# Optimization experiments

Hardware: AMD Instinct MI355X
Metric: run time of the kernel (lower is better)

Reference implementation:

```python
import jax, jax.numpy as jnp
import numpy as np

B, S, K, N, G = 4, 2048, 4096, 11008, 128  # batch, seq, in_features, out_features, groupsize


def setup_inputs() -> dict:
    key = jax.random.key(0)
    k1, k2, k3, k4 = jax.random.split(key, 4)
    x = jax.random.normal(k1, (B, S, K), dtype=jnp.float32)
    # unpacked int4 codes in [0, 16)
    weight_q = jax.random.randint(k2, (N, K), 0, 16, dtype=jnp.int32)
    # groupwise scales (positive, small) and zeros, packed as [K//G, N, 2]
    scales = jax.random.uniform(k3, (K // G, N), dtype=jnp.float32) * 0.02 + 1e-3
    zeros = jax.random.normal(k4, (K // G, N), dtype=jnp.float32) * 0.1
    scales_and_zeros = jnp.stack([scales, zeros], axis=-1)  # [K//G, N, 2]
    return {"x": x, "weight_q": weight_q, "scales_and_zeros": scales_and_zeros}


def reference(x, weight_q, scales_and_zeros):
    # Dequantize groupwise: w[n,k] = (q[n,k] - 8) * scale[k//G, n] + zero[k//G, n]
    scales = scales_and_zeros[..., 0].T  # [N, K//G]
    zeros = scales_and_zeros[..., 1].T   # [N, K//G]
    q = weight_q.astype(x.dtype).reshape(N, K // G, G)  # [N, K//G, G]
    w = (q - 8.0) * scales[:, :, None] + zeros[:, :, None]  # fused dequant
    w = w.reshape(N, K)
    # y[b,s,n] = sum_k x[b,s,k] * w[n,k]
    return jnp.einsum("bsk,nk->bsn", x, w)
```

## Files before the change

kernel.cpp:

```cpp
#include <hip/hip_runtime.h>
#include <stdint.h>


typedef __attribute__((ext_vector_type(8))) short short8;
typedef __attribute__((ext_vector_type(4))) float float4v;
typedef __attribute__((ext_vector_type(4))) int int4v;
typedef __attribute__((ext_vector_type(2))) float float2v;
typedef __attribute__((ext_vector_type(4))) unsigned short ushort4v;

static constexpr int M_ = 8192;
static constexpr int K_ = 4096;
static constexpr int N_ = 11008;
static constexpr int NKT = K_ / 64;

__device__ __forceinline__ unsigned short f2bf(float f) {
    union { float f; uint32_t u; } v;
    v.f = f;
    uint32_t u = v.u;
    u += 0x7fffu + ((u >> 16) & 1u);
    return (unsigned short)(u >> 16);
}

__device__ __forceinline__ void gload16(const void* g, void* l) {
    __builtin_amdgcn_global_load_lds(
        (const __attribute__((address_space(1))) uint32_t*)g,
        (__attribute__((address_space(3))) uint32_t*)l, 16, 0, 0);
}

__global__ __launch_bounds__(256) void cvt_x_kernel(const float* __restrict__ X,
                                                    unsigned short* __restrict__ Xb) {
    const int i = blockIdx.x * 256 + threadIdx.x;
    const float4v a = ((const float4v*)X)[2 * (size_t)i];
    const float4v b = ((const float4v*)X)[2 * (size_t)i + 1];
    short8 o;
    #pragma unroll
    for (int j = 0; j < 4; ++j) o[j] = (short)f2bf(a[j]);
    #pragma unroll
    for (int j = 0; j < 4; ++j) o[4 + j] = (short)f2bf(b[j]);
    ((short8*)Xb)[(size_t)i] = o;
}

__global__ __launch_bounds__(256) void deq_w_kernel(const int* __restrict__ Q,
                                                    const float* __restrict__ SZ,
                                                    unsigned short* __restrict__ Wb) {
    const int i = blockIdx.x * 256 + threadIdx.x;
    const int n = i >> 9;
    const int c = i & 511;
    const int k0 = c * 8;
    const int g = k0 >> 7;
    const float2v sz = *(const float2v*)(SZ + ((size_t)g * N_ + n) * 2);
    const float s = sz[0], z = sz[1];
    const int4v q0 = *(const int4v*)(Q + (size_t)n * K_ + k0);
    const int4v q1 = *(const int4v*)(Q + (size_t)n * K_ + k0 + 4);
    short8 o;
    #pragma unroll
    for (int j = 0; j < 4; ++j) o[j] = (short)f2bf((float)(q0[j] - 8) * s + z);
    #pragma unroll
    for (int j = 0; j < 4; ++j) o[4 + j] = (short)f2bf((float)(q1[j] - 8) * s + z);
    ((short8*)Wb)[(size_t)i] = o;
}


template <int BUF, int MH>
__device__ __forceinline__ void read_a(const char* ldsB, short8 (&a)[4][2],
                                       int aK0, int aK1) {
    constexpr int base = BUF * 32768 + MH * 16384;
    #pragma unroll
    for (int i = 0; i < 4; ++i) {
        a[i][0] = *(const short8*)(ldsB + base + i * 2048 + aK0);
        a[i][1] = *(const short8*)(ldsB + base + i * 2048 + aK1);
    }
}

template <int BUF, int NH>
__device__ __forceinline__ void read_b(const char* ldsB, short8 (&b)[2][2],
                                       int bK0, int bK1) {
    constexpr int base = BUF * 32768 + NH * 16384;
    #pragma unroll
    for (int j = 0; j < 2; ++j) {
        b[j][0] = *(const short8*)(ldsB + base + j * 2048 + bK0);
        b[j][1] = *(const short8*)(ldsB + base + j * 2048 + bK1);
    }
}

template <int MH, int NH>
__device__ __forceinline__ void phase_mma(short8 (&a)[4][2], short8 (&b)[2][2],
                                          float4v (&acc)[8][4]) {
    __builtin_amdgcn_s_setprio(1);
    #pragma unroll
    for (int i = 0; i < 4; ++i)
        #pragma unroll
        for (int j = 0; j < 2; ++j) {
            acc[MH * 4 + i][NH * 2 + j] = __builtin_amdgcn_mfma_f32_16x16x32_bf16(
                a[i][0], b[j][0], acc[MH * 4 + i][NH * 2 + j], 0, 0, 0);
            acc[MH * 4 + i][NH * 2 + j] = __builtin_amdgcn_mfma_f32_16x16x32_bf16(
                a[i][1], b[j][1], acc[MH * 4 + i][NH * 2 + j], 0, 0, 0);
        }
    __builtin_amdgcn_s_setprio(0);
}

#define SBAR() __builtin_amdgcn_sched_barrier(0)
#define VMW(n) asm volatile("s_waitcnt vmcnt(" #n ")" ::: "memory")

__global__ __launch_bounds__(512, 2) void gemm_bf16_8ph(
    const unsigned short* __restrict__ Agl,
    const unsigned short* __restrict__ Bgl,
    float* __restrict__ C) {
    __shared__ alignas(16) unsigned short lds[65536];

    const int tid = threadIdx.x;
    const int lane = tid & 63;
    const int wid = tid >> 6;
    const int wr = wid >> 2;
    const int wc = wid & 3;

    const int bid = blockIdx.x;
    const int wg = (bid & 7) * 172 + (bid >> 3);
    const int mt = wg / 43;
    const int nt = wg % 43;
    const int row0 = mt * 256;
    const int col0 = nt * 256;

    const int r8 = lane >> 3;
    const int kc = ((lane & 7) ^ r8) * 8;

    const int l15 = lane & 15;
    const int k0o = ((lane >> 4) * 16) ^ ((l15 & 7) << 4);
    const int k1o = k0o ^ 64;
    const int aK0 = (wr * 64 + l15) * 128 + k0o;
    const int aK1 = (wr * 64 + l15) * 128 + k1o;
    const int bK0 = 65536 + (wc * 32 + l15) * 128 + k0o;
    const int bK1 = 65536 + (wc * 32 + l15) * 128 + k1o;
    const char* ldsB = (const char*)lds;
    unsigned short* ldsU = lds;
    const char* AglB = (const char*)Agl;
    const char* BglB = (const char*)Bgl;

    uint32_t sA[2][2], sB[2][2];
    #pragma unroll
    for (int h = 0; h < 2; ++h)
        #pragma unroll
        for (int i = 0; i < 2; ++i) {
            sA[h][i] = (uint32_t)(row0 + h * 128 + (wid * 2 + i) * 8 + r8) * (K_ * 2)
                       + (uint32_t)kc * 2;
            sB[h][i] = (uint32_t)(col0 + h * 128 + (wid * 2 + i) * 8 + r8) * (K_ * 2)
                       + (uint32_t)kc * 2;
        }

    auto gA = [&](uint32_t& off, int b, int h, int i) {
        gload16(AglB + off, ldsU + b * 16384 + (h * 128 + (wid * 2 + i) * 8) * 64);
        off += 128;
    };
    auto gB = [&](uint32_t& off, int b, int h, int i) {
        gload16(BglB + off, ldsU + 32768 + b * 16384 + (h * 128 + (wid * 2 + i) * 8) * 64);
        off += 128;
    };

    float4v acc[8][4] = {};
    short8 a0[4][2], a1[4][2];
    short8 b0[2][2], b1[2][2];

    gA(sA[0][0], 0, 0, 0); gA(sA[0][1], 0, 0, 1);
    gA(sA[1][0], 0, 1, 0); gA(sA[1][1], 0, 1, 1);
    gB(sB[0][0], 0, 0, 0); gB(sB[0][1], 0, 0, 1);
    gB(sB[1][0], 0, 1, 0); gB(sB[1][1], 0, 1, 1);
    gA(sA[0][0], 1, 0, 0); gA(sA[0][1], 1, 0, 1);
    VMW(2);
    __builtin_amdgcn_s_barrier();
    SBAR();
    read_a<0, 0>(ldsB, a0, aK0, aK1);
    read_b<0, 0>(ldsB, b0, bK0, bK1);

#define KTILE(BUF, DN, DN2, MIDW, ENDW)                                    \
    {                                                                      \
        read_a<BUF, 1>(ldsB, a1, aK0, aK1);                                \
        if (DN) {                                                          \
            gA(sA[1][0], (BUF) ^ 1, 1, 0); gA(sA[1][1], (BUF) ^ 1, 1, 1);  \
            gB(sB[0][0], (BUF) ^ 1, 0, 0); gB(sB[0][1], (BUF) ^ 1, 0, 1);  \
        }                                                                  \
        phase_mma<0, 0>(a0, b0, acc);                                      \
        read_b<BUF, 1>(ldsB, b1, bK0, bK1);                                \
        if (DN) { gB(sB[1][0], (BUF) ^ 1, 1, 0); gB(sB[1][1], (BUF) ^ 1, 1, 1); } \
        phase_mma<1, 0>(a1, b0, acc);                                      \
        if (DN2) { gA(sA[0][0], BUF, 0, 0); gA(sA[0][1], BUF, 0, 1); }     \
        if (DN) {                                                          \
            SBAR(); VMW(MIDW);                                             \
            __builtin_amdgcn_s_barrier(); SBAR();                          \
            read_b<(BUF) ^ 1, 0>(ldsB, b0, bK0, bK1);                      \
        }                                                                  \
        phase_mma<0, 1>(a0, b1, acc);                                      \
        if (DN) read_a<(BUF) ^ 1, 0>(ldsB, a0, aK0, aK1);                  \
        phase_mma<1, 1>(a1, b1, acc);                                      \
        if (DN) {                                                          \
            SBAR(); VMW(ENDW);                                             \
            __builtin_amdgcn_s_barrier(); SBAR();                          \
        }                                                                  \
    }

    for (int t2 = 0; t2 < NKT - 2; t2 += 2) {
        KTILE(0, 1, 1, 4, 2);
        KTILE(1, 1, 1, 4, 2);
    }
    KTILE(0, 1, 0, 2, 0);
    KTILE(1, 0, 0, 0, 0);
#undef KTILE

    const int lrow = (lane >> 4) * 4;
    #pragma unroll
    for (int mf = 0; mf < 8; ++mf)
        #pragma unroll
        for (int nf = 0; nf < 4; ++nf)
            #pragma unroll
            for (int j = 0; j < 4; ++j) {
                const int r = row0 + (mf >> 2) * 128 + wr * 64 + (mf & 3) * 16 + lrow + j;
                const int c = col0 + (nf >> 1) * 128 + wc * 32 + (nf & 1) * 16 + l15;
                C[(size_t)r * N_ + c] = acc[mf][nf][j];
            }
}

static constexpr int LDSS = 40;

__global__ __launch_bounds__(256, 2) void w4_gemm_fused(
    const float* __restrict__ X, const int* __restrict__ Q,
    const float* __restrict__ SZ, float* __restrict__ C) {
    __shared__ alignas(16) unsigned short As[128 * LDSS];
    __shared__ alignas(16) unsigned short Ws[128 * LDSS];
    const int tid = threadIdx.x;
    const int lane = tid & 63;
    const int wid = tid >> 6;
    const int wrr = wid >> 1;
    const int wcc = wid & 1;
    const int row0 = blockIdx.x * 128;
    const int col0 = blockIdx.y * 128;
    float4v acc[4][4] = {};
    float4v a_reg[4];
    int4v q_reg[4];
    float2v sz_reg[4];

    auto load_tile = [&](int kb) {
        const int g = kb >> 7;
        #pragma unroll
        for (int i = 0; i < 4; ++i) {
            const int idx = tid + 256 * i;
            const int r = idx >> 3;
            const int v = idx & 7;
            a_reg[i] = *(const float4v*)(X + (size_t)(row0 + r) * K_ + kb + v * 4);
            q_reg[i] = *(const int4v*)(Q + (size_t)(col0 + r) * K_ + kb + v * 4);
            sz_reg[i] = *(const float2v*)(SZ + ((size_t)g * N_ + (col0 + r)) * 2);
        }
    };
    auto write_tile = [&]() {
        #pragma unroll
        for (int i = 0; i < 4; ++i) {
            const int idx = tid + 256 * i;
            const int r = idx >> 3;
            const int v = idx & 7;
            ushort4v ab, wb;
            #pragma unroll
            for (int j = 0; j < 4; ++j) ab[j] = f2bf(a_reg[i][j]);
            const float s = sz_reg[i][0];
            const float z = sz_reg[i][1];
            #pragma unroll
            for (int j = 0; j < 4; ++j) wb[j] = f2bf((float)(q_reg[i][j] - 8) * s + z);
            *(ushort4v*)(&As[r * LDSS + v * 4]) = ab;
            *(ushort4v*)(&Ws[r * LDSS + v * 4]) = wb;
        }
    };
    auto compute = [&]() {
        const int lr = lane & 15;
        const int lg = lane >> 4;
        short8 af[4], bf[4];
        #pragma unroll
        for (int mf = 0; mf < 4; ++mf)
            af[mf] = *(const short8*)(&As[(wrr * 64 + mf * 16 + lr) * LDSS + lg * 8]);
        #pragma unroll
        for (int nf = 0; nf < 4; ++nf)
            bf[nf] = *(const short8*)(&Ws[(wcc * 64 + nf * 16 + lr) * LDSS + lg * 8]);
        #pragma unroll
        for (int mf = 0; mf < 4; ++mf)
            #pragma unroll
            for (int nf = 0; nf < 4; ++nf)
                acc[mf][nf] = __builtin_amdgcn_mfma_f32_16x16x32_bf16(
                    af[mf], bf[nf], acc[mf][nf], 0, 0, 0);
    };

    load_tile(0);
    for (int kb = 0; kb < K_; kb += 32) {
        __syncthreads();
        write_tile();
        __syncthreads();
        if (kb + 32 < K_) load_tile(kb + 32);
        compute();
    }
    const int lr = lane & 15;
    const int lg = lane >> 4;
    #pragma unroll
    for (int mf = 0; mf < 4; ++mf)
        #pragma unroll
        for (int nf = 0; nf < 4; ++nf)
            #pragma unroll
            for (int j = 0; j < 4; ++j) {
                const int r = row0 + wrr * 64 + mf * 16 + lg * 4 + j;
                const int c = col0 + wcc * 64 + nf * 16 + lr;
                C[(size_t)r * N_ + c] = acc[mf][nf][j];
            }
}

extern "C" void kernel_launch(void* const* d_in, const int* in_sizes, int n_in,
                              void* d_out, int out_size, void* d_ws, size_t ws_size,
                              hipStream_t stream) {
    const float* X  = (const float*)d_in[0];
    const int*   Q  = (const int*)d_in[1];
    const float* SZ = (const float*)d_in[2];
    float* C = (float*)d_out;

    const size_t xb_bytes = (size_t)M_ * K_ * 2;
    const size_t wb_bytes = (size_t)N_ * K_ * 2;
    if (ws_size >= xb_bytes + wb_bytes) {
        unsigned short* Xb = (unsigned short*)d_ws;
        unsigned short* Wb = (unsigned short*)((char*)d_ws + xb_bytes);
        cvt_x_kernel<<<(M_ * (K_ / 8)) / 256, 256, 0, stream>>>(X, Xb);
        deq_w_kernel<<<(N_ * (K_ / 8)) / 256, 256, 0, stream>>>(Q, SZ, Wb);
        gemm_bf16_8ph<<<dim3(1376), dim3(512), 0, stream>>>(Xb, Wb, C);
    } else {
        dim3 grid(M_ / 128, N_ / 128);
        w4_gemm_fused<<<grid, dim3(256), 0, stream>>>(X, Q, SZ, C);
    }
}
```

Measured before the change: 802.5 us.

## Restructure bf16 GEMM K-loop into barrier-separated phases with explicit lgkm waits

Replaces the cross-tile register-prefetch pipeline in the bf16 GEMM main loop with a per-tile schedule. Each tile reads its A/B fragments from LDS, then issues global-to-LDS loads for the next buffer, with extra workgroup barriers and explicit lgkmcnt waits between the four MFMA phases. The aim is to interleave global loads, LDS reads and MFMA more regularly across the waves. It adds many more barriers per K tile and drops the register-level prefetch across tiles, which may expose LDS latency.

```diff
diff --git a/kernel.cpp b/kernel.cpp
--- a/kernel.cpp
+++ b/kernel.cpp
@@ -101,6 +101,8 @@
 
 #define SBAR() __builtin_amdgcn_sched_barrier(0)
 #define VMW(n) asm volatile("s_waitcnt vmcnt(" #n ")" ::: "memory")
+#define LGKM(n) asm volatile("s_waitcnt lgkmcnt(" #n ")" ::: "memory")
+#define BARRIER() __builtin_amdgcn_s_barrier()
 
 __global__ __launch_bounds__(512, 2) void gemm_bf16_8ph(
     const unsigned short* __restrict__ Agl,
@@ -157,52 +159,57 @@
     };
 
     float4v acc[8][4] = {};
-    short8 a0[4][2], a1[4][2];
-    short8 b0[2][2], b1[2][2];
 
     gA(sA[0][0], 0, 0, 0); gA(sA[0][1], 0, 0, 1);
-    gA(sA[1][0], 0, 1, 0); gA(sA[1][1], 0, 1, 1);
     gB(sB[0][0], 0, 0, 0); gB(sB[0][1], 0, 0, 1);
     gB(sB[1][0], 0, 1, 0); gB(sB[1][1], 0, 1, 1);
-    gA(sA[0][0], 1, 0, 0); gA(sA[0][1], 1, 0, 1);
-    VMW(2);
-    __builtin_amdgcn_s_barrier();
-    SBAR();
-    read_a<0, 0>(ldsB, a0, aK0, aK1);
-    read_b<0, 0>(ldsB, b0, bK0, bK1);
-
-#define KTILE(BUF, DN, DN2, MIDW, ENDW)                                    \
-    {                                                                      \
-        read_a<BUF, 1>(ldsB, a1, aK0, aK1);                                \
-        if (DN) {                                                          \
-            gA(sA[1][0], (BUF) ^ 1, 1, 0); gA(sA[1][1], (BUF) ^ 1, 1, 1);  \
-            gB(sB[0][0], (BUF) ^ 1, 0, 0); gB(sB[0][1], (BUF) ^ 1, 0, 1);  \
-        }                                                                  \
-        phase_mma<0, 0>(a0, b0, acc);                                      \
-        read_b<BUF, 1>(ldsB, b1, bK0, bK1);                                \
+    gA(sA[1][0], 0, 1, 0); gA(sA[1][1], 0, 1, 1);
+    VMW(4);
+    BARRIER(); SBAR();
+
+#define KTILE(BUF, DN, W1, W2, W3, DOEND)                                   \
+    {                                                                       \
+        short8 a0[4][2], a1[4][2], b0[2][2], b1[2][2];                      \
+                                   \
+        read_a<BUF, 0>(ldsB, a0, aK0, aK1);                                 \
+        read_b<BUF, 0>(ldsB, b0, bK0, bK1);                                 \
+        if (DN) { gA(sA[0][0], (BUF) ^ 1, 0, 0); gA(sA[0][1], (BUF) ^ 1, 0, 1); } \
+        LGKM(8);                                                            \
+        BARRIER(); SBAR();                                                  \
+        LGKM(0); SBAR();                                                    \
+        phase_mma<0, 0>(a0, b0, acc);                                       \
+        VMW(W1);                                                            \
+        BARRIER(); SBAR();                                                  \
+                                       \
+        read_b<BUF, 1>(ldsB, b1, bK0, bK1);                                 \
+        if (DN) { gB(sB[0][0], (BUF) ^ 1, 0, 0); gB(sB[0][1], (BUF) ^ 1, 0, 1); } \
+        BARRIER(); SBAR();                                                  \
+        LGKM(0); SBAR();                                                    \
+        phase_mma<0, 1>(a0, b1, acc);                                       \
+        VMW(W2);                                                            \
+        BARRIER(); SBAR();                                                  \
+                                       \
+        read_a<BUF, 1>(ldsB, a1, aK0, aK1);                                 \
         if (DN) { gB(sB[1][0], (BUF) ^ 1, 1, 0); gB(sB[1][1], (BUF) ^ 1, 1, 1); } \
-        phase_mma<1, 0>(a1, b0, acc);                                      \
-        if (DN2) { gA(sA[0][0], BUF, 0, 0); gA(sA[0][1], BUF, 0, 1); }     \
-        if (DN) {                                                          \
-            SBAR(); VMW(MIDW);                                             \
-            __builtin_amdgcn_s_barrier(); SBAR();                          \
-            read_b<(BUF) ^ 1, 0>(ldsB, b0, bK0, bK1);                      \
-        }                                                                  \
-        phase_mma<0, 1>(a0, b1, acc);                                      \
-        if (DN) read_a<(BUF) ^ 1, 0>(ldsB, a0, aK0, aK1);                  \
-        phase_mma<1, 1>(a1, b1, acc);                                      \
-        if (DN) {                                                          \
-            SBAR(); VMW(ENDW);                                             \
-            __builtin_amdgcn_s_barrier(); SBAR();                          \
-        }                                                                  \
+        BARRIER(); SBAR();                                                  \
+        LGKM(0); SBAR();                                                    \
+        phase_mma<1, 0>(a1, b0, acc);                                       \
+        BARRIER(); SBAR();                                                  \
+                                          \
+        if (DN) { gA(sA[1][0], (BUF) ^ 1, 1, 0); gA(sA[1][1], (BUF) ^ 1, 1, 1); } \
+        phase_mma<1, 1>(a1, b1, acc);                                       \
+        if (DOEND) {                                                        \
+            VMW(W3);                                                        \
+            BARRIER(); SBAR();                                              \
+        }                                                                   \
     }
 
     for (int t2 = 0; t2 < NKT - 2; t2 += 2) {
-        KTILE(0, 1, 1, 4, 2);
-        KTILE(1, 1, 1, 4, 2);
-    }
-    KTILE(0, 1, 0, 2, 0);
-    KTILE(1, 0, 0, 0, 0);
+        KTILE(0, 1, 4, 4, 4, 1);
+        KTILE(1, 1, 4, 4, 4, 1);
+    }
+    KTILE(0, 1, 4, 4, 4, 1);
+    KTILE(1, 0, 2, 0, 0, 0);
 #undef KTILE
 
     const int lrow = (lane >> 4) * 4;
```

Measured after the change: 750.4 us. 6.5% less time.
